# Kernel optimization log

Hardware: AMD Instinct MI355X
Metric: run time of the kernel (lower is better)

## Reference

```python
import jax, jax.numpy as jnp
import numpy as np

B, S, D = 1, 2048, 2048
H = 16            # num query heads
QL = 1536         # q_lora_rank
KVL = 512         # kv_lora_rank
DN = 128          # qk_nope_head_dim
DR = 64           # qk_rope_head_dim
DV = 128          # v_head_dim
F = 8192          # ffn intermediate
EPS = 1e-6
WAVE = 10000.0


def _rms(x, scale, eps=EPS):
    # fp32 norm then cast back, matching DeepSeekV3_1RMSNorm
    x32 = x.astype(jnp.float32)
    ms = jnp.mean(x32 * x32, axis=-1, keepdims=True)
    return (x32 * jax.lax.rsqrt(ms + eps)).astype(x.dtype) * scale


def _rope_tables(seq_len, dim):
    inv_freq = 1.0 / (WAVE ** (jnp.arange(0, dim, 2, dtype=jnp.float32) / dim))
    t = jnp.arange(seq_len, dtype=jnp.float32)[:, None] * inv_freq[None, :]  # [S, dim/2]
    emb = jnp.concatenate([t, t], axis=-1)  # [S, dim]
    return jnp.cos(emb), jnp.sin(emb)


def _apply_rope(x, cos, sin):
    # x: [B, S, H, dr]; rotate-half convention
    half = x.shape[-1] // 2
    x1, x2 = x[..., :half], x[..., half:]
    rot = jnp.concatenate([-x2, x1], axis=-1)
    return x * cos[None, :, None, :] + rot * sin[None, :, None, :]


def setup_inputs() -> dict:
    key = jax.random.key(0)
    ks = jax.random.split(key, 12)
    w = lambda k, shp: (jax.random.normal(k, shp, dtype=jnp.float32) * 0.02)
    inp = {
        "hidden_states": jax.random.normal(ks[0], (B, S, D), dtype=jnp.float32),
        "attention_mask": jnp.broadcast_to(jnp.tril(jnp.ones((S, S), dtype=bool)), (B, S, S)),
        "pre_attn_scale": jnp.ones((D,), jnp.float32),
        "wqa": w(ks[1], (D, QL)),
        "q_norm_scale": jnp.ones((QL,), jnp.float32),
        "wqb": w(ks[2], (QL, H * (DN + DR))),
        "wkva": w(ks[3], (D, KVL + DR)),
        "kv_norm_scale": jnp.ones((KVL,), jnp.float32),
        "wkvb": w(ks[4], (KVL, H * (DN + DV))),
        "wo": w(ks[5], (H * DV, D)),
        "pre_ffn_scale": jnp.ones((D,), jnp.float32),
        "wg": w(ks[6], (D, F)),
        "bg": jnp.zeros((F,), jnp.float32),
        "wu": w(ks[7], (D, F)),
        "bu": jnp.zeros((F,), jnp.float32),
        "wd": w(ks[8], (F, D)),
        "bd": jnp.zeros((D,), jnp.float32),
    }
    return inp


def reference(hidden_states, attention_mask, pre_attn_scale, wqa, q_norm_scale, wqb,
              wkva, kv_norm_scale, wkvb, wo, pre_ffn_scale, wg, bg, wu, bu, wd, bd):
    x = hidden_states
    # --- pre-attention RMSNorm ---
    n = _rms(x, pre_attn_scale)
    # --- MLA attention ---
    q = (_rms(n @ wqa, q_norm_scale) @ wqb).reshape(B, S, H, DN + DR)
    q_nope, q_rope = q[..., :DN], q[..., DN:]
    kva = n @ wkva                              # [B,S,KVL+DR]
    c_kv, k_rope = kva[..., :KVL], kva[..., KVL:]
    kv = (_rms(c_kv, kv_norm_scale) @ wkvb).reshape(B, S, H, DN + DV)
    k_nope, v = kv[..., :DN], kv[..., DN:]
    cos, sin = _rope_tables(S, DR)
    q_rope = _apply_rope(q_rope, cos, sin)
    k_rope = _apply_rope(k_rope[:, :, None, :], cos, sin)  # [B,S,1,DR] shared across heads
    qf = jnp.concatenate([q_nope, q_rope], axis=-1)
    kf = jnp.concatenate([k_nope, jnp.broadcast_to(k_rope, (B, S, H, DR))], axis=-1)
    scale = 1.0 / float(np.sqrt(DN + DR))
    scores = jnp.einsum('bqhd,bkhd->bhqk', qf, kf) * scale
    scores = jnp.where(attention_mask[:, None, :, :], scores, jnp.float32(-1e9))
    probs = jax.nn.softmax(scores, axis=-1)
    attn = jnp.einsum('bhqk,bkhd->bqhd', probs, v).reshape(B, S, H * DV)
    x = x + attn @ wo                            # residual 1 (dropout=0)
    # --- pre-FFN RMSNorm + dense SwiGLU FFN ---
    n = _rms(x, pre_ffn_scale)
    ff = (jax.nn.silu(n @ wg + bg) * (n @ wu + bu)) @ wd + bd
    return x + ff                                # residual 2
```

## Files before the change

kernel.cpp:

```cpp
#include <hip/hip_runtime.h>
#include <hip/hip_bf16.h>
#include <stdint.h>

typedef unsigned short u16;
using f32x4  = __attribute__((ext_vector_type(4))) float;
using bf16x8 = __attribute__((ext_vector_type(8))) __bf16;
using u32x4  = __attribute__((ext_vector_type(4))) uint32_t;
using u16x4  = __attribute__((ext_vector_type(4))) unsigned short;
using u16x8  = __attribute__((ext_vector_type(8))) unsigned short;

#define S_LEN 2048
#define DM    2048
#define NH    16
#define QLR   1536
#define KVLR  512
#define DNOPE 128
#define DROPE 64
#define DVAL  128
#define FFD   8192

static __device__ __forceinline__ float bf2f(u16 u) {
    union { uint32_t i; float f; } v; v.i = ((uint32_t)u) << 16; return v.f;
}
static __device__ __forceinline__ u16 f2bf(float f) {
    union { float f; uint32_t i; } v; v.f = f;
    uint32_t x = v.i;
    return (u16)((x + 0x7FFF + ((x >> 16) & 1)) >> 16);
}
static __device__ __forceinline__ void gload16(const u16* g, const u16* l) {
    __builtin_amdgcn_global_load_lds(
        (const __attribute__((address_space(1))) void*)g,
        (__attribute__((address_space(3))) void*)l, 16, 0, 0);
}

struct TWJob { const float* src; u16* dst; int R, C, xt, start; };
struct TWJobs { TWJob j[8]; };

__global__ __launch_bounds__(256)
void transpose_all(TWJobs jobs)
{
    __shared__ __align__(16) u16 tile[64][68];
    const int bid = blockIdx.x;
    int e = 0;
#pragma unroll
    for (int i = 1; i < 8; ++i) e = (bid >= jobs.j[i].start) ? i : e;
    const float* src = jobs.j[e].src;
    u16* dst = jobs.j[e].dst;
    const int R = jobs.j[e].R, C = jobs.j[e].C;
    const int local = bid - jobs.j[e].start;
    const int c0 = (local % jobs.j[e].xt) * 64;
    const int r0 = (local / jobs.j[e].xt) * 64;
    const int t = threadIdx.x;
#pragma unroll
    for (int i = 0; i < 4; ++i) {
        int idx = i * 256 + t;
        int r = idx >> 4, c4 = idx & 15;
        float4 v = *reinterpret_cast<const float4*>(&src[(size_t)(r0 + r) * C + c0 + c4 * 4]);
        u16x4 b; b[0] = f2bf(v.x); b[1] = f2bf(v.y); b[2] = f2bf(v.z); b[3] = f2bf(v.w);
        *reinterpret_cast<u16x4*>(&tile[r][c4 * 4]) = b;
    }
    __syncthreads();
#pragma unroll
    for (int i = 0; i < 4; ++i) {
        int idx = i * 256 + t;
        int rr = idx >> 4, k4 = idx & 15;
        u16x4 o;
#pragma unroll
        for (int j = 0; j < 4; ++j) o[j] = tile[k4 * 4 + j][rr];
        *reinterpret_cast<u16x4*>(&dst[(size_t)(c0 + rr) * R + r0 + k4 * 4]) = o;
    }
}

__global__ __launch_bounds__(256)
void transpose_v(const u16* __restrict__ kv, u16* __restrict__ vt)
{
    __shared__ __align__(16) u16 tile[64][76];
    const int t = threadIdx.x;
    const int s0 = blockIdx.x * 64;
    const int d0 = blockIdx.y * 64;
    const int h  = blockIdx.z;
#pragma unroll
    for (int i = 0; i < 2; ++i) {
        int idx = i * 256 + t;
        int s = idx >> 3, c8 = idx & 7;
        u16x8 v = *reinterpret_cast<const u16x8*>(kv + (size_t)(s0 + s) * (NH * 256) + h * 256 + 128 + d0 + c8 * 8);
        u16x4 lo, hi;
#pragma unroll
        for (int j = 0; j < 4; ++j) { lo[j] = v[j]; hi[j] = v[4 + j]; }
        *reinterpret_cast<u16x4*>(&tile[s][c8 * 8])     = lo;
        *reinterpret_cast<u16x4*>(&tile[s][c8 * 8 + 4]) = hi;
    }
    __syncthreads();
#pragma unroll
    for (int i = 0; i < 4; ++i) {
        int idx = i * 256 + t;
        int d = idx >> 4, s4 = idx & 15;
        u16x4 o;
#pragma unroll
        for (int j = 0; j < 4; ++j) o[j] = tile[s4 * 4 + j][d];
        *reinterpret_cast<u16x4*>(&vt[(size_t)(h * 128 + d0 + d) * S_LEN + s0 + s4 * 4]) = o;
    }
}

template<bool IN_F32>
__global__ __launch_bounds__(256)
void rms_norm(const void* __restrict__ in, int in_stride, int width,
              const float* __restrict__ scale, u16* __restrict__ out, int out_stride)
{
    const int row = blockIdx.x;
    const int t = threadIdx.x;
    const float* inf = (const float*)in;
    const u16*   inb = (const u16*)in;
    float ss = 0.f;
    for (int c = t; c < width; c += 256) {
        float v = IN_F32 ? inf[(size_t)row * in_stride + c] : bf2f(inb[(size_t)row * in_stride + c]);
        ss += v * v;
    }
#pragma unroll
    for (int o = 32; o > 0; o >>= 1) ss += __shfl_xor(ss, o);
    __shared__ float red[4];
    if ((t & 63) == 0) red[t >> 6] = ss;
    __syncthreads();
    float inv = rsqrtf((red[0] + red[1] + red[2] + red[3]) / (float)width + 1e-6f);
    for (int c = t; c < width; c += 256) {
        float v = IN_F32 ? inf[(size_t)row * in_stride + c] : bf2f(inb[(size_t)row * in_stride + c]);
        out[(size_t)row * out_stride + c] = f2bf(v * inv * scale[c]);
    }
}

__global__ __launch_bounds__(256)
void rope_qk(u16* __restrict__ q, const u16* __restrict__ kva, u16* __restrict__ kr)
{
    const int s = blockIdx.x;
    const int t = threadIdx.x;
    for (int idx = t; idx < 544; idx += 256) {
        int d = idx & 31;
        float invf = powf(10000.f, -(float)(2 * d) / 64.f);
        float ang = (float)s * invf;
        float cs = cosf(ang), sn = sinf(ang);
        if (idx < 512) {
            int hh = idx >> 5;
            u16* base = q + ((size_t)s * NH + hh) * 192 + 128;
            float x1 = bf2f(base[d]), x2 = bf2f(base[d + 32]);
            base[d]      = f2bf(x1 * cs - x2 * sn);
            base[d + 32] = f2bf(x2 * cs + x1 * sn);
        } else {
            const u16* kb = kva + (size_t)s * 576 + 512;
            float x1 = bf2f(kb[d]), x2 = bf2f(kb[d + 32]);
            kr[(size_t)s * 64 + d]      = f2bf(x1 * cs - x2 * sn);
            kr[(size_t)s * 64 + d + 32] = f2bf(x2 * cs + x1 * sn);
        }
    }
}

__global__ __launch_bounds__(256)
void init_out(const float* __restrict__ x2, const float* __restrict__ bd,
              float* __restrict__ out, int total4, int N)
{
    int i = blockIdx.x * 256 + threadIdx.x;
    const int stride = gridDim.x * 256;
    for (; i < total4; i += stride) {
        float4 r = ((const float4*)x2)[i];
        int col = (i * 4) & (N - 1);
        float4 b = *reinterpret_cast<const float4*>(&bd[col]);
        float4 o; o.x = r.x + b.x; o.y = r.y + b.y; o.z = r.z + b.z; o.w = r.w + b.w;
        ((float4*)out)[i] = o;
    }
}

template<int EPI>
__global__ __launch_bounds__(256)
void gemm_bt(const u16* __restrict__ A, const u16* __restrict__ BT,
             void* __restrict__ out, int M, int N, int K)
{
    __shared__ __align__(16) u16 As[128 * 64];
    __shared__ __align__(16) u16 Bs[128 * 64];
    const int t = threadIdx.x;
    const int lane = t & 63;
    const int w = t >> 6;
    const int wr = w >> 1, wc = w & 1;
    const int li = lane & 15;
    const int lg = lane >> 4;

    const int gx = gridDim.x;
    int nwg = gx * gridDim.y;
    int bid = blockIdx.y * gx + blockIdx.x;
    bid = (bid & 7) * (nwg >> 3) + (bid >> 3);
    const int m0 = (bid % gx) * 128;
    const int n0 = (bid / gx) * 128;

    const int srow = w * 32 + (lane >> 3);
    const int scol = (((lane & 7) ^ (lane >> 3)) << 3);
    const u16* ag = A  + (size_t)(m0 + srow) * K + scol;
    const u16* bg = BT + (size_t)(n0 + srow) * K + scol;

    f32x4 acc[4][4];
#pragma unroll
    for (int m = 0; m < 4; ++m)
#pragma unroll
        for (int n = 0; n < 4; ++n)
            acc[m][n] = f32x4{0.f, 0.f, 0.f, 0.f};

    const int nkt = K >> 6;
    for (int kt = 0; kt < nkt; ++kt) {
        const int k0 = kt << 6;
        __syncthreads();
#pragma unroll
        for (int i = 0; i < 4; ++i) {
            gload16(ag + (size_t)i * 8 * K + k0, As + (w * 32 + i * 8) * 64);
            gload16(bg + (size_t)i * 8 * K + k0, Bs + (w * 32 + i * 8) * 64);
        }
        __syncthreads();
#pragma unroll
        for (int kk = 0; kk < 2; ++kk) {
            const int csw = (kk * 32 + lg * 8) ^ ((li & 7) << 3);
            bf16x8 af[4], bfr[4];
#pragma unroll
            for (int m = 0; m < 4; ++m)
                af[m] = *reinterpret_cast<const bf16x8*>(As + (wr * 64 + m * 16 + li) * 64 + csw);
#pragma unroll
            for (int n = 0; n < 4; ++n)
                bfr[n] = *reinterpret_cast<const bf16x8*>(Bs + (wc * 64 + n * 16 + li) * 64 + csw);
#pragma unroll
            for (int m = 0; m < 4; ++m)
#pragma unroll
                for (int n = 0; n < 4; ++n)
                    acc[m][n] = __builtin_amdgcn_mfma_f32_16x16x32_bf16(af[m], bfr[n], acc[m][n], 0, 0, 0);
        }
    }

#pragma unroll
    for (int m = 0; m < 4; ++m) {
        const int row = m0 + wr * 64 + m * 16 + lg * 4;
#pragma unroll
        for (int n = 0; n < 4; ++n) {
            const int col = n0 + wc * 64 + n * 16 + li;
            if (col < N) {
#pragma unroll
                for (int r2 = 0; r2 < 4; ++r2)
                    ((u16*)out)[(size_t)(row + r2) * N + col] = f2bf(acc[m][n][r2]);
            }
        }
    }
}

template<int EPI>
__global__ __launch_bounds__(512, 2)
void gemm_big(const u16* __restrict__ A, const u16* __restrict__ BT,
              void* __restrict__ out, int M, int N, int K,
              const float* __restrict__ bias, const u16* __restrict__ gmul)
{
    __shared__ __align__(16) u16 As[2][256 * 64];
    __shared__ __align__(16) u16 Bs[2][128 * 64];
    const int t = threadIdx.x;
    const int lane = t & 63;
    const int w = t >> 6;
    const int wr = w >> 1, wc = w & 1;
    const int li = lane & 15;
    const int lg = lane >> 4;

    const int gx = gridDim.x;
    int nwg = gx * gridDim.y;
    int bid = blockIdx.y * gx + blockIdx.x;
    bid = (bid & 7) * (nwg >> 3) + (bid >> 3);
    const int m0 = (bid % gx) * 256;
    const int n0 = (bid / gx) * 128;

    const int nz = gridDim.z, z = blockIdx.z;
    const int nktt = K >> 6;
    const int qq = nktt / nz, rr = nktt % nz;
    const int kt0 = z * qq + (z < rr ? z : rr);
    const int ktEnd = kt0 + qq + (z < rr ? 1 : 0);

    const int sr = lane >> 3;
    const int scol = (((lane & 7) ^ sr) << 3);
    const u16* ag = A  + (size_t)(m0 + w * 8 + sr) * K + scol;
    const u16* bg = BT + (size_t)(n0 + w * 8 + sr) * K + scol;

    auto stage = [&](int b, int kt) {
        const int k0 = kt << 6;
        u16* lA = &As[b][(w * 8) * 64];
        u16* lB = &Bs[b][(w * 8) * 64];
#pragma unroll
        for (int i = 0; i < 4; ++i)
            gload16(ag + (size_t)i * 64 * K + k0, lA + i * 64 * 64);
#pragma unroll
        for (int i = 0; i < 2; ++i)
            gload16(bg + (size_t)i * 64 * K + k0, lB + i * 64 * 64);
    };

    f32x4 acc[4][4];
#pragma unroll
    for (int m = 0; m < 4; ++m)
#pragma unroll
        for (int n = 0; n < 4; ++n)
            acc[m][n] = f32x4{0.f, 0.f, 0.f, 0.f};

    stage(0, kt0);
    if (kt0 + 1 < ktEnd) stage(1, kt0 + 1);

    for (int kt = kt0; kt < ktEnd; ++kt) {
        const int cur = (kt - kt0) & 1;
        if (kt + 1 < ktEnd) asm volatile("s_waitcnt vmcnt(6)" ::: "memory");
        else                asm volatile("s_waitcnt vmcnt(0)" ::: "memory");
        __builtin_amdgcn_s_barrier();
        __builtin_amdgcn_sched_barrier(0);

        bf16x8 af[2][4], bfr[2][4];
#pragma unroll
        for (int kk = 0; kk < 2; ++kk) {
            const int csw = (kk * 32 + lg * 8) ^ ((li & 7) << 3);
#pragma unroll
            for (int m = 0; m < 4; ++m)
                af[kk][m] = *reinterpret_cast<const bf16x8*>(&As[cur][(wr * 64 + m * 16 + li) * 64 + csw]);
#pragma unroll
            for (int n = 0; n < 4; ++n)
                bfr[kk][n] = *reinterpret_cast<const bf16x8*>(&Bs[cur][(wc * 64 + n * 16 + li) * 64 + csw]);
        }
        asm volatile("s_waitcnt lgkmcnt(0)" ::: "memory");
        __builtin_amdgcn_sched_barrier(0);
        __builtin_amdgcn_s_barrier();
        __builtin_amdgcn_sched_barrier(0);

        if (kt + 2 < ktEnd) stage(cur, kt + 2);

        __builtin_amdgcn_s_setprio(1);
#pragma unroll
        for (int kk = 0; kk < 2; ++kk)
#pragma unroll
            for (int m = 0; m < 4; ++m)
#pragma unroll
                for (int n = 0; n < 4; ++n)
                    acc[m][n] = __builtin_amdgcn_mfma_f32_16x16x32_bf16(af[kk][m], bfr[kk][n], acc[m][n], 0, 0, 0);
        __builtin_amdgcn_s_setprio(0);
    }

#pragma unroll
    for (int m = 0; m < 4; ++m) {
        const int row = m0 + wr * 64 + m * 16 + lg * 4;
#pragma unroll
        for (int n = 0; n < 4; ++n) {
            const int col = n0 + wc * 64 + n * 16 + li;
#pragma unroll
            for (int r2 = 0; r2 < 4; ++r2) {
                float v = acc[m][n][r2];
                size_t idx = (size_t)(row + r2) * N + col;
                if (EPI == 0) {
                    ((u16*)out)[idx] = f2bf(v);
                } else if (EPI == 1) {
                    v += bias[col];
                    v = v / (1.f + __expf(-v));
                    ((u16*)out)[idx] = f2bf(v);
                } else if (EPI == 2) {
                    v = (v + bias[col]) * bf2f(gmul[idx]);
                    ((u16*)out)[idx] = f2bf(v);
                } else {
                    unsafeAtomicAdd((float*)out + idx, v);
                }
            }
        }
    }
}

__global__ __launch_bounds__(256)
void flash_attn(const u16* __restrict__ q, const u16* __restrict__ kv,
                const u16* __restrict__ kr, const u16* __restrict__ vt,
                u16* __restrict__ attn)
{
    __shared__ __align__(16) u16 KVs[2][20480];
    __shared__ __align__(16) u16 Ps[4][16][72];

    const int t = threadIdx.x;
    const int lane = t & 63;
    const int w = t >> 6;
    const int li = lane & 15;
    const int lg = lane >> 4;
    const int h = blockIdx.x;
    const int by = blockIdx.y;

    const int qtp[2]  = {31 - by, by};
    const int nktp[2] = {32 - by, by + 1};

    auto stage = [&](int buf, int k0) {
        u16* base = &KVs[buf][0];
#pragma unroll
        for (int i = 0; i < 6; ++i) {
            int g = w * 6 + i;
            int P = g * 64 + lane;
            int j = P / 24, s = P % 24;
            int c = (s & 24) | ((s ^ (j & 7)) & 7);
            const u16* src = (c < 16)
                ? kv + (size_t)(k0 + j) * (NH * 256) + h * 256 + c * 8
                : kr + (size_t)(k0 + j) * 64 + (c - 16) * 8;
            gload16(src, base + g * 512);
        }
#pragma unroll
        for (int i = 0; i < 4; ++i) {
            int g = w * 4 + i;
            int P = g * 64 + lane;
            int d = P >> 3, s8 = P & 7;
            int c = s8 ^ (d & 7);
            const u16* src = vt + (size_t)(h * 128 + d) * S_LEN + k0 + c * 8;
            gload16(src, base + 12288 + g * 512);
        }
    };

    stage(0, 0);
    int buf = 0;
    const float scale = 0.07216878364870322f;

    for (int pass = 0; pass < 2; ++pass) {
        const int qt = qtp[pass];
        const int nkt = nktp[pass];
        const int qr = qt * 64 + w * 16;
        const int qpos = qr + li;

        bf16x8 qf[6];
#pragma unroll
        for (int kb = 0; kb < 6; ++kb)
            qf[kb] = *reinterpret_cast<const bf16x8*>(q + ((size_t)(qr + li) * NH + h) * 192 + kb * 32 + lg * 8);

        f32x4 oacc[8];
#pragma unroll
        for (int i = 0; i < 8; ++i) oacc[i] = f32x4{0.f, 0.f, 0.f, 0.f};
        float m_run = -INFINITY, l_run = 0.f;

        for (int kt = 0; kt < nkt; ++kt) {
            const int k0 = kt << 6;
            __syncthreads();
            if (kt + 1 < nkt)       stage(buf ^ 1, (kt + 1) << 6);
            else if (pass == 0)     stage(buf ^ 1, 0);

            const u16* bb = &KVs[buf][0];

            f32x4 sacc[4];
#pragma unroll
            for (int jt = 0; jt < 4; ++jt) sacc[jt] = f32x4{0.f, 0.f, 0.f, 0.f};
            __builtin_amdgcn_s_setprio(1);
#pragma unroll
            for (int kb = 0; kb < 6; ++kb) {
                const int c = kb * 4 + lg;
                const int s = (c & 24) | ((c ^ (li & 7)) & 7);
#pragma unroll
                for (int jt = 0; jt < 4; ++jt) {
                    bf16x8 kf = *reinterpret_cast<const bf16x8*>(bb + ((jt * 16 + li) * 24 + s) * 8);
                    sacc[jt] = __builtin_amdgcn_mfma_f32_16x16x32_bf16(kf, qf[kb], sacc[jt], 0, 0, 0);
                }
            }
            __builtin_amdgcn_s_setprio(0);

            float p[16];
            float mt = -INFINITY;
            if (k0 + 63 <= qr) {
#pragma unroll
                for (int jt = 0; jt < 4; ++jt)
#pragma unroll
                    for (int r = 0; r < 4; ++r) {
                        float sv = sacc[jt][r] * scale;
                        p[jt * 4 + r] = sv;
                        mt = fmaxf(mt, sv);
                    }
            } else {
#pragma unroll
                for (int jt = 0; jt < 4; ++jt)
#pragma unroll
                    for (int r = 0; r < 4; ++r) {
                        int jpos = k0 + jt * 16 + lg * 4 + r;
                        float sv = (jpos <= qpos) ? sacc[jt][r] * scale : -INFINITY;
                        p[jt * 4 + r] = sv;
                        mt = fmaxf(mt, sv);
                    }
            }
            mt = fmaxf(mt, __shfl_xor(mt, 16));
            mt = fmaxf(mt, __shfl_xor(mt, 32));
            if (!__all(mt <= m_run + 8.f)) {
                float mn = fmaxf(m_run, mt);
                float sf = __expf(m_run - mn);
                float sfr[4];
#pragma unroll
                for (int r = 0; r < 4; ++r)
                    sfr[r] = __shfl(sf, (lane & 48) + lg * 4 + r);
#pragma unroll
                for (int d2 = 0; d2 < 8; ++d2)
#pragma unroll
                    for (int r = 0; r < 4; ++r)
                        oacc[d2][r] *= sfr[r];
                l_run *= sf;
                m_run = mn;
            }
            float rsum = 0.f;
#pragma unroll
            for (int i2 = 0; i2 < 16; ++i2) { p[i2] = __expf(p[i2] - m_run); rsum += p[i2]; }
            rsum += __shfl_xor(rsum, 16);
            rsum += __shfl_xor(rsum, 32);
            l_run += rsum;

#pragma unroll
            for (int jt = 0; jt < 4; ++jt) {
                u16x4 pk;
                pk[0] = f2bf(p[jt * 4 + 0]); pk[1] = f2bf(p[jt * 4 + 1]);
                pk[2] = f2bf(p[jt * 4 + 2]); pk[3] = f2bf(p[jt * 4 + 3]);
                *reinterpret_cast<u16x4*>(&Ps[w][li][jt * 16 + lg * 4]) = pk;
            }

            __builtin_amdgcn_s_setprio(1);
#pragma unroll
            for (int ks = 0; ks < 2; ++ks) {
                bf16x8 pf = *reinterpret_cast<const bf16x8*>(&Ps[w][li][ks * 32 + lg * 8]);
                const int vs = (ks * 4 + lg) ^ (li & 7);
#pragma unroll
                for (int d2 = 0; d2 < 8; ++d2) {
                    bf16x8 vf = *reinterpret_cast<const bf16x8*>(bb + 12288 + ((d2 * 16 + li) * 8 + vs) * 8);
                    oacc[d2] = __builtin_amdgcn_mfma_f32_16x16x32_bf16(pf, vf, oacc[d2], 0, 0, 0);
                }
            }
            __builtin_amdgcn_s_setprio(0);
            buf ^= 1;
        }

        float rl = 1.f / l_run;
        float rlr[4];
#pragma unroll
        for (int r = 0; r < 4; ++r)
            rlr[r] = __shfl(rl, (lane & 48) + lg * 4 + r);
#pragma unroll
        for (int d2 = 0; d2 < 8; ++d2)
#pragma unroll
            for (int r = 0; r < 4; ++r) {
                int srow = qr + lg * 4 + r;
                int dcol = d2 * 16 + li;
                attn[(size_t)srow * (NH * DVAL) + h * DVAL + dcol] = f2bf(oacc[d2][r] * rlr[r]);
            }
    }
}

extern "C" void kernel_launch(void* const* d_in, const int* in_sizes, int n_in,
                              void* d_out, int out_size, void* d_ws, size_t ws_size,
                              hipStream_t stream)
{
    const float* hidden   = (const float*)d_in[0];
    const float* pa_scale = (const float*)d_in[2];
    const float* wqa      = (const float*)d_in[3];
    const float* qn_scale = (const float*)d_in[4];
    const float* wqb      = (const float*)d_in[5];
    const float* wkva     = (const float*)d_in[6];
    const float* kv_scale = (const float*)d_in[7];
    const float* wkvb     = (const float*)d_in[8];
    const float* wo       = (const float*)d_in[9];
    const float* pf_scale = (const float*)d_in[10];
    const float* wg       = (const float*)d_in[11];
    const float* bg       = (const float*)d_in[12];
    const float* wu       = (const float*)d_in[13];
    const float* bu       = (const float*)d_in[14];
    const float* wd       = (const float*)d_in[15];
    const float* bd       = (const float*)d_in[16];
    float* out = (float*)d_out;

    size_t off = 0;
    auto alloc = [&](size_t bytes) {
        off = (off + 255) & ~(size_t)255;
        void* p = (char*)d_ws + off;
        off += bytes;
        return p;
    };
    u16* wqaT  = (u16*)alloc((size_t)QLR * DM * 2);
    u16* wqbT  = (u16*)alloc((size_t)3072 * QLR * 2);
    u16* wkvaT = (u16*)alloc((size_t)640 * DM * 2);
    u16* wkvbT = (u16*)alloc((size_t)4096 * KVLR * 2);
    u16* woT   = (u16*)alloc((size_t)DM * DM * 2);
    u16* wgT   = (u16*)alloc((size_t)FFD * DM * 2);
    u16* wuT   = (u16*)alloc((size_t)FFD * DM * 2);
    u16* wdT   = (u16*)alloc((size_t)DM * FFD * 2);
    u16* n1    = (u16*)alloc((size_t)S_LEN * DM * 2);
    u16* qlora = (u16*)alloc((size_t)S_LEN * QLR * 2);
    u16* qn    = (u16*)alloc((size_t)S_LEN * QLR * 2);
    u16* qbuf  = (u16*)alloc((size_t)S_LEN * 3072 * 2);
    u16* kva   = (u16*)alloc((size_t)S_LEN * 576 * 2);
    u16* ckvn  = (u16*)alloc((size_t)S_LEN * KVLR * 2);
    u16* kvbuf = (u16*)alloc((size_t)S_LEN * 4096 * 2);
    u16* krbuf = (u16*)alloc((size_t)S_LEN * 64 * 2);
    u16* attnb = (u16*)alloc((size_t)S_LEN * DM * 2);
    float* x2  = (float*)alloc((size_t)S_LEN * DM * 4);
    u16* n2    = (u16*)alloc((size_t)S_LEN * DM * 2);
    u16* gbuf  = (u16*)alloc((size_t)S_LEN * FFD * 2);
    u16* hbuf  = (u16*)alloc((size_t)S_LEN * FFD * 2);
    u16* vtb = qlora;
    (void)ws_size; (void)in_sizes; (void)n_in; (void)out_size;

    TWJobs jobs;
    int startAcc = 0;
    auto setJob = [&](int i, const float* s, u16* d, int R, int C) {
        jobs.j[i] = TWJob{s, d, R, C, C / 64, startAcc};
        startAcc += (C / 64) * (R / 64);
    };
    setJob(0, wqa,  wqaT,  2048, 1536);
    setJob(1, wqb,  wqbT,  1536, 3072);
    setJob(2, wkva, wkvaT, 2048,  576);
    setJob(3, wkvb, wkvbT,  512, 4096);
    setJob(4, wo,   woT,   2048, 2048);
    setJob(5, wg,   wgT,   2048, 8192);
    setJob(6, wu,   wuT,   2048, 8192);
    setJob(7, wd,   wdT,   8192, 2048);
    hipLaunchKernelGGL(transpose_all, dim3(startAcc), 256, 0, stream, jobs);

    hipLaunchKernelGGL((rms_norm<true>),  dim3(S_LEN), 256, 0, stream, hidden, DM, DM, pa_scale, n1, DM);

    hipLaunchKernelGGL((gemm_bt<0>), dim3(16, 12), 256, 0, stream, n1, wqaT, qlora, S_LEN, QLR, DM);
    hipLaunchKernelGGL((gemm_bt<0>), dim3(16,  5), 256, 0, stream, n1, wkvaT, kva, S_LEN, 576, DM);
    hipLaunchKernelGGL((rms_norm<false>), dim3(S_LEN), 256, 0, stream, qlora, QLR, QLR, qn_scale, qn, QLR);
    hipLaunchKernelGGL((gemm_bt<0>), dim3(16, 24), 256, 0, stream, qn, wqbT, qbuf, S_LEN, 3072, QLR);
    hipLaunchKernelGGL((rms_norm<false>), dim3(S_LEN), 256, 0, stream, kva, 576, KVLR, kv_scale, ckvn, KVLR);
    hipLaunchKernelGGL(rope_qk, dim3(S_LEN), 256, 0, stream, qbuf, kva, krbuf);
    hipLaunchKernelGGL((gemm_big<0>), dim3(8, 32), 512, 0, stream, ckvn, wkvbT, kvbuf, S_LEN, 4096, KVLR, nullptr, nullptr);

    hipLaunchKernelGGL(transpose_v, dim3(S_LEN/64, 2, NH), 256, 0, stream, kvbuf, vtb);
    hipLaunchKernelGGL(flash_attn, dim3(NH, 16), 256, 0, stream, qbuf, kvbuf, krbuf, vtb, attnb);

    hipMemcpyAsync(x2, hidden, (size_t)S_LEN * DM * 4, hipMemcpyDeviceToDevice, stream);
    hipLaunchKernelGGL((gemm_big<5>), dim3(8, 16, 4), 512, 0, stream, attnb, woT, x2, S_LEN, DM, DM, nullptr, nullptr);

    hipLaunchKernelGGL((rms_norm<true>), dim3(S_LEN), 256, 0, stream, x2, DM, DM, pf_scale, n2, DM);

    hipLaunchKernelGGL(init_out, dim3(2048), 256, 0, stream, x2, bd, out, S_LEN * DM / 4, DM);
    hipLaunchKernelGGL((gemm_big<1>), dim3(8, 64), 512, 0, stream, n2, wgT, gbuf, S_LEN, FFD, DM, bg, nullptr);
    hipLaunchKernelGGL((gemm_big<2>), dim3(8, 64), 512, 0, stream, n2, wuT, hbuf, S_LEN, FFD, DM, bu, gbuf);
    hipLaunchKernelGGL((gemm_big<5>), dim3(8, 16, 4), 512, 0, stream, hbuf, wdT, out, S_LEN, DM, FFD, nullptr, nullptr);
}
```

Measured before the change: 713.8 us.

## Split-K the small q/kv-down GEMMs with fp32 atomics and drop big-GEMM double buffering

```diff
diff --git a/kernel.cpp b/kernel.cpp
--- a/kernel.cpp
+++ b/kernel.cpp
@@ -129,7 +129,7 @@
 }
 
 __global__ __launch_bounds__(256)
-void rope_qk(u16* __restrict__ q, const u16* __restrict__ kva, u16* __restrict__ kr)
+void rope_qk(u16* __restrict__ q, const float* __restrict__ kva, u16* __restrict__ kr)
 {
     const int s = blockIdx.x;
     const int t = threadIdx.x;
@@ -145,8 +145,8 @@
             base[d]      = f2bf(x1 * cs - x2 * sn);
             base[d + 32] = f2bf(x2 * cs + x1 * sn);
         } else {
-            const u16* kb = kva + (size_t)s * 576 + 512;
-            float x1 = bf2f(kb[d]), x2 = bf2f(kb[d + 32]);
+            const float* kb = kva + (size_t)s * 576 + 512;
+            float x1 = kb[d], x2 = kb[d + 32];
             kr[(size_t)s * 64 + d]      = f2bf(x1 * cs - x2 * sn);
             kr[(size_t)s * 64 + d + 32] = f2bf(x2 * cs + x1 * sn);
         }
@@ -189,6 +189,12 @@
     const int m0 = (bid % gx) * 128;
     const int n0 = (bid / gx) * 128;
 
+    const int nz = gridDim.z, z = blockIdx.z;
+    const int nktt = K >> 6;
+    const int qq = nktt / nz, rr = nktt % nz;
+    const int kt0 = z * qq + (z < rr ? z : rr);
+    const int ktEnd = kt0 + qq + (z < rr ? 1 : 0);
+
     const int srow = w * 32 + (lane >> 3);
     const int scol = (((lane & 7) ^ (lane >> 3)) << 3);
     const u16* ag = A  + (size_t)(m0 + srow) * K + scol;
@@ -201,8 +207,7 @@
         for (int n = 0; n < 4; ++n)
             acc[m][n] = f32x4{0.f, 0.f, 0.f, 0.f};
 
-    const int nkt = K >> 6;
-    for (int kt = 0; kt < nkt; ++kt) {
+    for (int kt = kt0; kt < ktEnd; ++kt) {
         const int k0 = kt << 6;
         __syncthreads();
 #pragma unroll
@@ -237,21 +242,25 @@
             const int col = n0 + wc * 64 + n * 16 + li;
             if (col < N) {
 #pragma unroll
-                for (int r2 = 0; r2 < 4; ++r2)
-                    ((u16*)out)[(size_t)(row + r2) * N + col] = f2bf(acc[m][n][r2]);
+                for (int r2 = 0; r2 < 4; ++r2) {
+                    float v = acc[m][n][r2];
+                    size_t idx = (size_t)(row + r2) * N + col;
+                    if (EPI == 0) ((u16*)out)[idx] = f2bf(v);
+                    else          unsafeAtomicAdd((float*)out + idx, v);
+                }
             }
         }
     }
 }
 
 template<int EPI>
-__global__ __launch_bounds__(512, 2)
+__global__ __launch_bounds__(512, 4)
 void gemm_big(const u16* __restrict__ A, const u16* __restrict__ BT,
               void* __restrict__ out, int M, int N, int K,
               const float* __restrict__ bias, const u16* __restrict__ gmul)
 {
-    __shared__ __align__(16) u16 As[2][256 * 64];
-    __shared__ __align__(16) u16 Bs[2][128 * 64];
+    __shared__ __align__(16) u16 As[256 * 64];
+    __shared__ __align__(16) u16 Bs[128 * 64];
     const int t = threadIdx.x;
     const int lane = t & 63;
     const int w = t >> 6;
@@ -276,62 +285,43 @@
     const int scol = (((lane & 7) ^ sr) << 3);
     const u16* ag = A  + (size_t)(m0 + w * 8 + sr) * K + scol;
     const u16* bg = BT + (size_t)(n0 + w * 8 + sr) * K + scol;
-
-    auto stage = [&](int b, int kt) {
+    const u16* lA = As + (w * 8) * 64;
+    const u16* lB = Bs + (w * 8) * 64;
+
+    f32x4 acc[4][4];
+#pragma unroll
+    for (int m = 0; m < 4; ++m)
+#pragma unroll
+        for (int n = 0; n < 4; ++n)
+            acc[m][n] = f32x4{0.f, 0.f, 0.f, 0.f};
+
+    for (int kt = kt0; kt < ktEnd; ++kt) {
         const int k0 = kt << 6;
-        u16* lA = &As[b][(w * 8) * 64];
-        u16* lB = &Bs[b][(w * 8) * 64];
+        __syncthreads();
 #pragma unroll
         for (int i = 0; i < 4; ++i)
             gload16(ag + (size_t)i * 64 * K + k0, lA + i * 64 * 64);
 #pragma unroll
         for (int i = 0; i < 2; ++i)
             gload16(bg + (size_t)i * 64 * K + k0, lB + i * 64 * 64);
-    };
-
-    f32x4 acc[4][4];
-#pragma unroll
-    for (int m = 0; m < 4; ++m)
-#pragma unroll
-        for (int n = 0; n < 4; ++n)
-            acc[m][n] = f32x4{0.f, 0.f, 0.f, 0.f};
-
-    stage(0, kt0);
-    if (kt0 + 1 < ktEnd) stage(1, kt0 + 1);
-
-    for (int kt = kt0; kt < ktEnd; ++kt) {
-        const int cur = (kt - kt0) & 1;
-        if (kt + 1 < ktEnd) asm volatile("s_waitcnt vmcnt(6)" ::: "memory");
-        else                asm volatile("s_waitcnt vmcnt(0)" ::: "memory");
-        __builtin_amdgcn_s_barrier();
-        __builtin_amdgcn_sched_barrier(0);
-
-        bf16x8 af[2][4], bfr[2][4];
+        __syncthreads();
+        __builtin_amdgcn_s_setprio(1);
 #pragma unroll
         for (int kk = 0; kk < 2; ++kk) {
             const int csw = (kk * 32 + lg * 8) ^ ((li & 7) << 3);
+            bf16x8 af[4], bfr[4];
 #pragma unroll
             for (int m = 0; m < 4; ++m)
-                af[kk][m] = *reinterpret_cast<const bf16x8*>(&As[cur][(wr * 64 + m * 16 + li) * 64 + csw]);
+                af[m] = *reinterpret_cast<const bf16x8*>(As + (wr * 64 + m * 16 + li) * 64 + csw);
 #pragma unroll
             for (int n = 0; n < 4; ++n)
-                bfr[kk][n] = *reinterpret_cast<const bf16x8*>(&Bs[cur][(wc * 64 + n * 16 + li) * 64 + csw]);
-        }
-        asm volatile("s_waitcnt lgkmcnt(0)" ::: "memory");
-        __builtin_amdgcn_sched_barrier(0);
-        __builtin_amdgcn_s_barrier();
-        __builtin_amdgcn_sched_barrier(0);
-
-        if (kt + 2 < ktEnd) stage(cur, kt + 2);
-
-        __builtin_amdgcn_s_setprio(1);
-#pragma unroll
-        for (int kk = 0; kk < 2; ++kk)
+                bfr[n] = *reinterpret_cast<const bf16x8*>(Bs + (wc * 64 + n * 16 + li) * 64 + csw);
 #pragma unroll
             for (int m = 0; m < 4; ++m)
 #pragma unroll
                 for (int n = 0; n < 4; ++n)
-                    acc[m][n] = __builtin_amdgcn_mfma_f32_16x16x32_bf16(af[kk][m], bfr[kk][n], acc[m][n], 0, 0, 0);
+                    acc[m][n] = __builtin_amdgcn_mfma_f32_16x16x32_bf16(af[m], bfr[n], acc[m][n], 0, 0, 0);
+        }
         __builtin_amdgcn_s_setprio(0);
     }
 
@@ -572,10 +562,10 @@
     u16* wuT   = (u16*)alloc((size_t)FFD * DM * 2);
     u16* wdT   = (u16*)alloc((size_t)DM * FFD * 2);
     u16* n1    = (u16*)alloc((size_t)S_LEN * DM * 2);
-    u16* qlora = (u16*)alloc((size_t)S_LEN * QLR * 2);
+    float* qlora32 = (float*)alloc((size_t)S_LEN * QLR * 4);
+    float* kva32   = (float*)alloc((size_t)S_LEN * 576 * 4);
     u16* qn    = (u16*)alloc((size_t)S_LEN * QLR * 2);
     u16* qbuf  = (u16*)alloc((size_t)S_LEN * 3072 * 2);
-    u16* kva   = (u16*)alloc((size_t)S_LEN * 576 * 2);
     u16* ckvn  = (u16*)alloc((size_t)S_LEN * KVLR * 2);
     u16* kvbuf = (u16*)alloc((size_t)S_LEN * 4096 * 2);
     u16* krbuf = (u16*)alloc((size_t)S_LEN * 64 * 2);
@@ -584,7 +574,7 @@
     u16* n2    = (u16*)alloc((size_t)S_LEN * DM * 2);
     u16* gbuf  = (u16*)alloc((size_t)S_LEN * FFD * 2);
     u16* hbuf  = (u16*)alloc((size_t)S_LEN * FFD * 2);
-    u16* vtb = qlora;
+    u16* vtb = (u16*)qlora32;
     (void)ws_size; (void)in_sizes; (void)n_in; (void)out_size;
 
     TWJobs jobs;
@@ -603,14 +593,17 @@
     setJob(7, wd,   wdT,   8192, 2048);
     hipLaunchKernelGGL(transpose_all, dim3(startAcc), 256, 0, stream, jobs);
 
+    hipMemsetAsync(qlora32, 0, (size_t)S_LEN * QLR * 4, stream);
+    hipMemsetAsync(kva32,   0, (size_t)S_LEN * 576 * 4, stream);
+
     hipLaunchKernelGGL((rms_norm<true>),  dim3(S_LEN), 256, 0, stream, hidden, DM, DM, pa_scale, n1, DM);
 
-    hipLaunchKernelGGL((gemm_bt<0>), dim3(16, 12), 256, 0, stream, n1, wqaT, qlora, S_LEN, QLR, DM);
-    hipLaunchKernelGGL((gemm_bt<0>), dim3(16,  5), 256, 0, stream, n1, wkvaT, kva, S_LEN, 576, DM);
-    hipLaunchKernelGGL((rms_norm<false>), dim3(S_LEN), 256, 0, stream, qlora, QLR, QLR, qn_scale, qn, QLR);
+    hipLaunchKernelGGL((gemm_bt<5>), dim3(16, 12, 2), 256, 0, stream, n1, wqaT, qlora32, S_LEN, QLR, DM);
+    hipLaunchKernelGGL((gemm_bt<5>), dim3(16,  5, 4), 256, 0, stream, n1, wkvaT, kva32, S_LEN, 576, DM);
+    hipLaunchKernelGGL((rms_norm<true>), dim3(S_LEN), 256, 0, stream, qlora32, QLR, QLR, qn_scale, qn, QLR);
     hipLaunchKernelGGL((gemm_bt<0>), dim3(16, 24), 256, 0, stream, qn, wqbT, qbuf, S_LEN, 3072, QLR);
-    hipLaunchKernelGGL((rms_norm<false>), dim3(S_LEN), 256, 0, stream, kva, 576, KVLR, kv_scale, ckvn, KVLR);
-    hipLaunchKernelGGL(rope_qk, dim3(S_LEN), 256, 0, stream, qbuf, kva, krbuf);
+    hipLaunchKernelGGL((rms_norm<true>), dim3(S_LEN), 256, 0, stream, kva32, 576, KVLR, kv_scale, ckvn, KVLR);
+    hipLaunchKernelGGL(rope_qk, dim3(S_LEN), 256, 0, stream, qbuf, kva32, krbuf);
     hipLaunchKernelGGL((gemm_big<0>), dim3(8, 32), 512, 0, stream, ckvn, wkvbT, kvbuf, S_LEN, 4096, KVLR, nullptr, nullptr);
 
     hipLaunchKernelGGL(transpose_v, dim3(S_LEN/64, 2, NH), 256, 0, stream, kvbuf, vtb);
```

New measurement: 644.2 us. -9.8%, faster.
